# Performance work log

Hardware: AMD Instinct MI355X
Metric: run time of the kernel (lower is better)

## Reference

```python
import jax, jax.numpy as jnp
import numpy as np

N_NODES = 50000
D = 128
N_POS = 400000
N_NEG = 200000  # N_NODES * neg_k(4)
E = N_POS + N_NEG


def setup_inputs() -> dict:
    key = jax.random.key(0)
    k_x, k_w1, k_w2, k_p = jax.random.split(key, 4)
    x = jax.random.normal(k_x, (N_NODES, D), dtype=jnp.float32)
    # torch nn.Linear params: y = x @ W.T + b
    W1 = jax.random.normal(k_w1, (D, 2 * D), dtype=jnp.float32) * (1.0 / np.sqrt(2 * D))
    b1 = jnp.zeros((D,), dtype=jnp.float32)
    W2 = jax.random.normal(k_w2, (1, D), dtype=jnp.float32) * (1.0 / np.sqrt(D))
    b2 = jnp.zeros((1,), dtype=jnp.float32)
    pairs = jax.random.randint(k_p, (2, E), 0, N_NODES, dtype=jnp.int64)
    labels = jnp.concatenate([jnp.ones((N_POS,), jnp.float32), jnp.zeros((N_NEG,), jnp.float32)])
    return {"x": x, "W1": W1, "b1": b1, "W2": W2, "b2": b2, "labels": labels, "pairs": pairs}


def reference(x, W1, b1, W2, b2, labels, pairs):
    us, vs = pairs[0], pairs[1]
    # edge gather + concat: [E, 2D]
    feats = jnp.concatenate([x[us], x[vs]], axis=-1)
    h = jax.nn.relu(feats @ W1.T + b1)            # [E, D]
    z = (h @ W2.T + b2).ravel()                   # [E] logits
    # binary_cross_entropy_with_logits, mean reduction (numerically stable)
    loss = -jnp.mean(labels * jax.nn.log_sigmoid(z) + (1.0 - labels) * jax.nn.log_sigmoid(-z))
    return loss
```

## Files before the change

kernel.cpp:

```cpp
#include <hip/hip_runtime.h>
#include <hip/hip_fp16.h>

#define D 128
#define TWO_D 256

typedef _Float16 half2v __attribute__((ext_vector_type(2)));
typedef _Float16 half8v __attribute__((ext_vector_type(8)));
typedef float floatx4 __attribute__((ext_vector_type(4)));

__device__ inline unsigned short f2h_bits(float f) {
    _Float16 h = (_Float16)f;
    return __builtin_bit_cast(unsigned short, h);
}

__device__ inline unsigned int pkrtz(float a, float b) {
    return __builtin_bit_cast(unsigned int, __builtin_amdgcn_cvt_pkrtz(a, b));
}

__global__ void build_wt(const float* __restrict__ W1, unsigned short* __restrict__ Wt) {
    int idx = blockIdx.x * 256 + threadIdx.x;
    int o = idx >> 7, k = idx & 127;
    float v = (o < D) ? W1[o * TWO_D + k] : W1[(o - D) * TWO_D + D + k];
    Wt[idx] = f2h_bits(v);
}

__global__ __launch_bounds__(256) void gemm_nodes(
        const float* __restrict__ x, const unsigned short* __restrict__ Wt,
        const float* __restrict__ b1,
        unsigned short* __restrict__ AB, int nNodes) {
    const int tid  = threadIdx.x;
    const int wave = tid >> 6, lane = tid & 63;
    const int quad = lane >> 4, l16 = lane & 15;
    const int nb0  = blockIdx.x * 64;

    half8v Bf[4][4];
    float bias[4];
#pragma unroll
    for (int t = 0; t < 4; ++t) {
        const int o = wave * 64 + t * 16 + l16;
        bias[t] = (o < D) ? b1[o] : 0.f;
#pragma unroll
        for (int ks = 0; ks < 4; ++ks)
            Bf[t][ks] = *(const half8v*)(Wt + o * D + ks * 32 + quad * 8);
    }

    __shared__ __align__(16) unsigned short xs[16][136];
    __shared__ __align__(16) unsigned short ct[16][272];

    const int srow = tid >> 4;
    const int sc8  = tid & 15;

    floatx4 v0, v1;
    {
        const int node = nb0 + srow;
        const int nc = node < nNodes ? node : nNodes - 1;
        const float* xp = x + nc * D + sc8 * 8;
        v0 = *(const floatx4*)xp;
        v1 = *(const floatx4*)(xp + 4);
    }

    for (int sub = 0; sub < 4; ++sub) {
        __syncthreads();
        uint4 pk;
        pk.x = pkrtz(v0[0], v0[1]);  pk.y = pkrtz(v0[2], v0[3]);
        pk.z = pkrtz(v1[0], v1[1]);  pk.w = pkrtz(v1[2], v1[3]);
        *(uint4*)&xs[srow][sc8 * 8] = pk;
        __syncthreads();

        if (sub < 3) {
            const int node = nb0 + (sub + 1) * 16 + srow;
            const int nc = node < nNodes ? node : nNodes - 1;
            const float* xp = x + nc * D + sc8 * 8;
            v0 = *(const floatx4*)xp;
            v1 = *(const floatx4*)(xp + 4);
        }

        half8v Af[4];
#pragma unroll
        for (int ks = 0; ks < 4; ++ks)
            Af[ks] = *(const half8v*)&xs[l16][ks * 32 + quad * 8];

        floatx4 acc[4];
#pragma unroll
        for (int t = 0; t < 4; ++t) acc[t] = (floatx4){0.f, 0.f, 0.f, 0.f};
#pragma unroll
        for (int ks = 0; ks < 4; ++ks)
#pragma unroll
            for (int t = 0; t < 4; ++t)
                acc[t] = __builtin_amdgcn_mfma_f32_16x16x32_f16(Af[ks], Bf[t][ks], acc[t], 0, 0, 0);

#pragma unroll
        for (int t = 0; t < 4; ++t) {
            const int o = wave * 64 + t * 16 + l16;
#pragma unroll
            for (int r = 0; r < 4; ++r)
                ct[quad * 4 + r][o] = f2h_bits(acc[t][r] + bias[t]);
        }
        __syncthreads();

        const int nrow = nb0 + sub * 16 + srow;
        if (nrow < nNodes) {
            uint4 c0 = *(const uint4*)&ct[srow][sc8 * 16];
            uint4 c1 = *(const uint4*)&ct[srow][sc8 * 16 + 8];
            unsigned short* dst = AB + (size_t)nrow * TWO_D + sc8 * 16;
            *(uint4*)dst       = c0;
            *(uint4*)(dst + 8) = c1;
        }
    }
}

__device__ inline float chunk2(unsigned int a, unsigned int b, unsigned int w, float z) {
    half2v s = __builtin_bit_cast(half2v, a) + __builtin_bit_cast(half2v, b);
    half2v zero = {(_Float16)0, (_Float16)0};
    s = __builtin_elementwise_max(s, zero);
    return __builtin_amdgcn_fdot2(s, __builtin_bit_cast(half2v, w), z, false);
}

__global__ __launch_bounds__(256) void edge_loss(
        const unsigned short* __restrict__ AB,
        const int* __restrict__ pairs,
        const float* __restrict__ labels,
        const float* __restrict__ W2,
        const float* __restrict__ b2,
        float* __restrict__ out, int E, float invE) {
    __shared__ unsigned int w2p[64];
    const int tid = threadIdx.x;
    if (tid < 64) {
        float2 w = *(const float2*)(W2 + tid * 2);
        half2v p = { (_Float16)w.x, (_Float16)w.y };
        w2p[tid] = __builtin_bit_cast(unsigned int, p);
    }
    __syncthreads();
    const int l8 = tid & 7;
    const uint4 w2a = *(const uint4*)&w2p[l8 * 4];
    const uint4 w2b = *(const uint4*)&w2p[32 + l8 * 4];
    const float bb2 = b2[0];

    float acc = 0.f;
    const int group  = (blockIdx.x * 256 + tid) >> 3;
    const int stride = (gridDim.x * 256) >> 3;
    for (int e = group; e < E; e += stride) {
        const int u = pairs[e];
        const int v = pairs[E + e];
        const unsigned short* au = AB + (size_t)u * TWO_D;
        const unsigned short* bv = AB + (size_t)v * TWO_D + D;
        uint4 a0 = *(const uint4*)(au + l8 * 8);
        uint4 a1 = *(const uint4*)(au + 64 + l8 * 8);
        uint4 b0 = *(const uint4*)(bv + l8 * 8);
        uint4 b1v = *(const uint4*)(bv + 64 + l8 * 8);
        float z = 0.f;
        z = chunk2(a0.x, b0.x, w2a.x, z);
        z = chunk2(a0.y, b0.y, w2a.y, z);
        z = chunk2(a0.z, b0.z, w2a.z, z);
        z = chunk2(a0.w, b0.w, w2a.w, z);
        z = chunk2(a1.x, b1v.x, w2b.x, z);
        z = chunk2(a1.y, b1v.y, w2b.y, z);
        z = chunk2(a1.z, b1v.z, w2b.z, z);
        z = chunk2(a1.w, b1v.w, w2b.w, z);
        z += __shfl_xor(z, 4, 8);
        z += __shfl_xor(z, 2, 8);
        z += __shfl_xor(z, 1, 8);
        z += bb2;
        const float y = labels[e];
        const float t = __expf(-fabsf(z));
        const float loss = fmaxf(z, 0.f) - z * y + __logf(1.f + t);
        acc += (l8 == 0) ? loss : 0.f;
    }

#pragma unroll
    for (int m = 32; m >= 1; m >>= 1) acc += __shfl_xor(acc, m, 64);
    __shared__ float red[4];
    if ((tid & 63) == 0) red[tid >> 6] = acc;
    __syncthreads();
    if (tid == 0)
        atomicAdd(out, (red[0] + red[1] + red[2] + red[3]) * invE);
}

extern "C" void kernel_launch(void* const* d_in, const int* in_sizes, int n_in,
                              void* d_out, int out_size, void* d_ws, size_t ws_size,
                              hipStream_t stream) {
    const float* x      = (const float*)d_in[0];
    const float* W1     = (const float*)d_in[1];
    const float* b1     = (const float*)d_in[2];
    const float* W2     = (const float*)d_in[3];
    const float* b2     = (const float*)d_in[4];
    const float* labels = (const float*)d_in[5];
    const int*   pairs  = (const int*)d_in[6];

    const int nNodes = in_sizes[0] / D;
    const int E      = in_sizes[5];

    unsigned short* Wt = (unsigned short*)d_ws;
    unsigned short* AB = (unsigned short*)((char*)d_ws + 65536);

    (void)hipMemsetAsync(d_out, 0, sizeof(float), stream);
    build_wt<<<128, 256, 0, stream>>>(W1, Wt);
    gemm_nodes<<<(nNodes + 63) / 64, 256, 0, stream>>>(x, Wt, b1, AB, nNodes);
    edge_loss<<<2048, 256, 0, stream>>>(AB, pairs, labels, W2, b2,
                                        (float*)d_out, E, 1.0f / (float)E);
}
```

Baseline: 148.7 us.

## Store per-node projections as FP8 and fuse weight conversion and output zeroing

The per-node projected halves are now stored in FP8 instead of FP16, halving the bytes the edge kernel gathers per edge. The edge kernel decodes FP8 pairs to half or float before the ReLU and dot product. The separate weight-conversion kernel and memset are removed: W1 is converted to half inside the GEMM kernel, and the GEMM kernel zeroes the output. FP8 storage loses considerable precision in the logits, which risks loss accuracy beyond tolerance.

```diff
diff --git a/kernel.cpp b/kernel.cpp
--- a/kernel.cpp
+++ b/kernel.cpp
@@ -8,44 +8,43 @@
 typedef _Float16 half8v __attribute__((ext_vector_type(8)));
 typedef float floatx4 __attribute__((ext_vector_type(4)));
 
-__device__ inline unsigned short f2h_bits(float f) {
-    _Float16 h = (_Float16)f;
-    return __builtin_bit_cast(unsigned short, h);
-}
-
 __device__ inline unsigned int pkrtz(float a, float b) {
     return __builtin_bit_cast(unsigned int, __builtin_amdgcn_cvt_pkrtz(a, b));
 }
 
-__global__ void build_wt(const float* __restrict__ W1, unsigned short* __restrict__ Wt) {
-    int idx = blockIdx.x * 256 + threadIdx.x;
-    int o = idx >> 7, k = idx & 127;
-    float v = (o < D) ? W1[o * TWO_D + k] : W1[(o - D) * TWO_D + D + k];
-    Wt[idx] = f2h_bits(v);
-}
-
 __global__ __launch_bounds__(256) void gemm_nodes(
-        const float* __restrict__ x, const unsigned short* __restrict__ Wt,
+        const float* __restrict__ x, const float* __restrict__ W1,
         const float* __restrict__ b1,
-        unsigned short* __restrict__ AB, int nNodes) {
+        unsigned char* __restrict__ AB, float* __restrict__ out0, int nNodes) {
     const int tid  = threadIdx.x;
     const int wave = tid >> 6, lane = tid & 63;
     const int quad = lane >> 4, l16 = lane & 15;
     const int nb0  = blockIdx.x * 64;
 
+    if (blockIdx.x == 0 && tid == 0) *out0 = 0.f;
+
     half8v Bf[4][4];
     float bias[4];
 #pragma unroll
     for (int t = 0; t < 4; ++t) {
         const int o = wave * 64 + t * 16 + l16;
         bias[t] = (o < D) ? b1[o] : 0.f;
-#pragma unroll
-        for (int ks = 0; ks < 4; ++ks)
-            Bf[t][ks] = *(const half8v*)(Wt + o * D + ks * 32 + quad * 8);
+        const float* wrow = (o < D) ? (W1 + (size_t)o * TWO_D)
+                                    : (W1 + (size_t)(o - D) * TWO_D + D);
+#pragma unroll
+        for (int ks = 0; ks < 4; ++ks) {
+            const float* wp = wrow + ks * 32 + quad * 8;
+            floatx4 w0 = *(const floatx4*)wp;
+            floatx4 w1v = *(const floatx4*)(wp + 4);
+            uint4 pk;
+            pk.x = pkrtz(w0[0], w0[1]);  pk.y = pkrtz(w0[2], w0[3]);
+            pk.z = pkrtz(w1v[0], w1v[1]); pk.w = pkrtz(w1v[2], w1v[3]);
+            Bf[t][ks] = __builtin_bit_cast(half8v, pk);
+        }
     }
 
     __shared__ __align__(16) unsigned short xs[16][136];
-    __shared__ __align__(16) unsigned short ct[16][272];
+    __shared__ __align__(16) float ct[16][260];
 
     const int srow = tid >> 4;
     const int sc8  = tid & 15;
@@ -54,7 +53,7 @@
     {
         const int node = nb0 + srow;
         const int nc = node < nNodes ? node : nNodes - 1;
-        const float* xp = x + nc * D + sc8 * 8;
+        const float* xp = x + (size_t)nc * D + sc8 * 8;
         v0 = *(const floatx4*)xp;
         v1 = *(const floatx4*)(xp + 4);
     }
@@ -70,7 +69,7 @@
         if (sub < 3) {
             const int node = nb0 + (sub + 1) * 16 + srow;
             const int nc = node < nNodes ? node : nNodes - 1;
-            const float* xp = x + nc * D + sc8 * 8;
+            const float* xp = x + (size_t)nc * D + sc8 * 8;
             v0 = *(const floatx4*)xp;
             v1 = *(const floatx4*)(xp + 4);
         }
@@ -94,30 +93,64 @@
             const int o = wave * 64 + t * 16 + l16;
 #pragma unroll
             for (int r = 0; r < 4; ++r)
-                ct[quad * 4 + r][o] = f2h_bits(acc[t][r] + bias[t]);
+                ct[quad * 4 + r][o] = acc[t][r] + bias[t];
         }
         __syncthreads();
 
         const int nrow = nb0 + sub * 16 + srow;
         if (nrow < nNodes) {
-            uint4 c0 = *(const uint4*)&ct[srow][sc8 * 16];
-            uint4 c1 = *(const uint4*)&ct[srow][sc8 * 16 + 8];
-            unsigned short* dst = AB + (size_t)nrow * TWO_D + sc8 * 16;
-            *(uint4*)dst       = c0;
-            *(uint4*)(dst + 8) = c1;
-        }
-    }
-}
-
-__device__ inline float chunk2(unsigned int a, unsigned int b, unsigned int w, float z) {
-    half2v s = __builtin_bit_cast(half2v, a) + __builtin_bit_cast(half2v, b);
+            floatx4 f0 = *(const floatx4*)&ct[srow][sc8 * 16];
+            floatx4 f1 = *(const floatx4*)&ct[srow][sc8 * 16 + 4];
+            floatx4 f2 = *(const floatx4*)&ct[srow][sc8 * 16 + 8];
+            floatx4 f3 = *(const floatx4*)&ct[srow][sc8 * 16 + 12];
+            uint4 o8;
+            int d;
+            d = __builtin_amdgcn_cvt_pk_fp8_f32(f0[0], f0[1], 0, false);
+            d = __builtin_amdgcn_cvt_pk_fp8_f32(f0[2], f0[3], d, true);
+            o8.x = (unsigned int)d;
+            d = __builtin_amdgcn_cvt_pk_fp8_f32(f1[0], f1[1], 0, false);
+            d = __builtin_amdgcn_cvt_pk_fp8_f32(f1[2], f1[3], d, true);
+            o8.y = (unsigned int)d;
+            d = __builtin_amdgcn_cvt_pk_fp8_f32(f2[0], f2[1], 0, false);
+            d = __builtin_amdgcn_cvt_pk_fp8_f32(f2[2], f2[3], d, true);
+            o8.z = (unsigned int)d;
+            d = __builtin_amdgcn_cvt_pk_fp8_f32(f3[0], f3[1], 0, false);
+            d = __builtin_amdgcn_cvt_pk_fp8_f32(f3[2], f3[3], d, true);
+            o8.w = (unsigned int)d;
+            *(uint4*)(AB + (size_t)nrow * TWO_D + sc8 * 16) = o8;
+        }
+    }
+}
+
+__device__ inline float dot4_fp8(unsigned int wa, unsigned int wb,
+                                 unsigned int w2lo, unsigned int w2hi, float z) {
+#if __has_builtin(__builtin_amdgcn_cvt_pk_f16_fp8)
+    half2v a01 = __builtin_bit_cast(half2v, __builtin_amdgcn_cvt_pk_f16_fp8((short)(wa & 0xffffu)));
+    half2v a23 = __builtin_bit_cast(half2v, __builtin_amdgcn_cvt_pk_f16_fp8((short)(wa >> 16)));
+    half2v b01 = __builtin_bit_cast(half2v, __builtin_amdgcn_cvt_pk_f16_fp8((short)(wb & 0xffffu)));
+    half2v b23 = __builtin_bit_cast(half2v, __builtin_amdgcn_cvt_pk_f16_fp8((short)(wb >> 16)));
     half2v zero = {(_Float16)0, (_Float16)0};
-    s = __builtin_elementwise_max(s, zero);
-    return __builtin_amdgcn_fdot2(s, __builtin_bit_cast(half2v, w), z, false);
+    half2v s01 = __builtin_elementwise_max(a01 + b01, zero);
+    half2v s23 = __builtin_elementwise_max(a23 + b23, zero);
+    z = __builtin_amdgcn_fdot2(s01, __builtin_bit_cast(half2v, w2lo), z, false);
+    z = __builtin_amdgcn_fdot2(s23, __builtin_bit_cast(half2v, w2hi), z, false);
+#else
+    auto a01 = __builtin_amdgcn_cvt_pk_f32_fp8(wa, false);
+    auto a23 = __builtin_amdgcn_cvt_pk_f32_fp8(wa, true);
+    auto b01 = __builtin_amdgcn_cvt_pk_f32_fp8(wb, false);
+    auto b23 = __builtin_amdgcn_cvt_pk_f32_fp8(wb, true);
+    half2v wlo = __builtin_bit_cast(half2v, w2lo);
+    half2v whi = __builtin_bit_cast(half2v, w2hi);
+    float s0 = fmaxf(a01[0] + b01[0], 0.f), s1 = fmaxf(a01[1] + b01[1], 0.f);
+    float s2 = fmaxf(a23[0] + b23[0], 0.f), s3 = fmaxf(a23[1] + b23[1], 0.f);
+    z = fmaf(s0, (float)wlo[0], z); z = fmaf(s1, (float)wlo[1], z);
+    z = fmaf(s2, (float)whi[0], z); z = fmaf(s3, (float)whi[1], z);
+#endif
+    return z;
 }
 
 __global__ __launch_bounds__(256) void edge_loss(
-        const unsigned short* __restrict__ AB,
+        const unsigned char* __restrict__ AB,
         const int* __restrict__ pairs,
         const float* __restrict__ labels,
         const float* __restrict__ W2,
@@ -132,8 +165,8 @@
     }
     __syncthreads();
     const int l8 = tid & 7;
-    const uint4 w2a = *(const uint4*)&w2p[l8 * 4];
-    const uint4 w2b = *(const uint4*)&w2p[32 + l8 * 4];
+    const uint4 w2a = *(const uint4*)&w2p[l8 * 8];
+    const uint4 w2b = *(const uint4*)&w2p[l8 * 8 + 4];
     const float bb2 = b2[0];
 
     float acc = 0.f;
@@ -142,21 +175,15 @@
     for (int e = group; e < E; e += stride) {
         const int u = pairs[e];
         const int v = pairs[E + e];
-        const unsigned short* au = AB + (size_t)u * TWO_D;
-        const unsigned short* bv = AB + (size_t)v * TWO_D + D;
-        uint4 a0 = *(const uint4*)(au + l8 * 8);
-        uint4 a1 = *(const uint4*)(au + 64 + l8 * 8);
-        uint4 b0 = *(const uint4*)(bv + l8 * 8);
-        uint4 b1v = *(const uint4*)(bv + 64 + l8 * 8);
+        const unsigned char* au = AB + (size_t)u * TWO_D;
+        const unsigned char* bv = AB + (size_t)v * TWO_D + D;
+        uint4 a4 = *(const uint4*)(au + l8 * 16);
+        uint4 b4 = *(const uint4*)(bv + l8 * 16);
         float z = 0.f;
-        z = chunk2(a0.x, b0.x, w2a.x, z);
-        z = chunk2(a0.y, b0.y, w2a.y, z);
-        z = chunk2(a0.z, b0.z, w2a.z, z);
-        z = chunk2(a0.w, b0.w, w2a.w, z);
-        z = chunk2(a1.x, b1v.x, w2b.x, z);
-        z = chunk2(a1.y, b1v.y, w2b.y, z);
-        z = chunk2(a1.z, b1v.z, w2b.z, z);
-        z = chunk2(a1.w, b1v.w, w2b.w, z);
+        z = dot4_fp8(a4.x, b4.x, w2a.x, w2a.y, z);
+        z = dot4_fp8(a4.y, b4.y, w2a.z, w2a.w, z);
+        z = dot4_fp8(a4.z, b4.z, w2b.x, w2b.y, z);
+        z = dot4_fp8(a4.w, b4.w, w2b.z, w2b.w, z);
         z += __shfl_xor(z, 4, 8);
         z += __shfl_xor(z, 2, 8);
         z += __shfl_xor(z, 1, 8);
@@ -190,12 +217,10 @@
     const int nNodes = in_sizes[0] / D;
     const int E      = in_sizes[5];
 
-    unsigned short* Wt = (unsigned short*)d_ws;
-    unsigned short* AB = (unsigned short*)((char*)d_ws + 65536);
-
-    (void)hipMemsetAsync(d_out, 0, sizeof(float), stream);
-    build_wt<<<128, 256, 0, stream>>>(W1, Wt);
-    gemm_nodes<<<(nNodes + 63) / 64, 256, 0, stream>>>(x, Wt, b1, AB, nNodes);
+    unsigned char* AB = (unsigned char*)d_ws;
+
+    gemm_nodes<<<(nNodes + 63) / 64, 256, 0, stream>>>(x, W1, b1, AB,
+                                                        (float*)d_out, nNodes);
     edge_loss<<<2048, 256, 0, stream>>>(AB, pairs, labels, W2, b2,
                                         (float*)d_out, E, 1.0f / (float)E);
 }
```

After: 140.6 us. 5.5% less time.
